# Optimization experiments

Hardware: AMD Instinct MI355X
Metric: run time of the kernel (lower is better)

Reference implementation:

```python
import jax, jax.numpy as jnp
import numpy as np
import math

B, S, IN_DIM = 4, 2048, 512
D, H, L, FF = 256, 4, 4, 2048
HD = D // H
EPS = 1e-5


def _pos_encoding(S, D, dtype=jnp.float32):
    pos = jnp.arange(S, dtype=jnp.float32)[:, None]
    div = jnp.exp(jnp.arange(0, D, 2, dtype=jnp.float32) * (-math.log(10000.0) / D))
    pe = jnp.zeros((S, D), dtype=jnp.float32)
    pe = pe.at[:, 0::2].set(jnp.sin(pos * div))
    pe = pe.at[:, 1::2].set(jnp.cos(pos * div))
    return pe.astype(dtype)


def _layernorm(x, w, b):
    mu = jnp.mean(x, axis=-1, keepdims=True)
    var = jnp.var(x, axis=-1, keepdims=True)
    return (x - mu) * jax.lax.rsqrt(var + EPS) * w + b


def setup_inputs() -> dict:
    key = jax.random.key(0)
    ks = jax.random.split(key, 12)
    sc = 0.02
    inp = {
        "x": jax.random.normal(ks[0], (B, S, IN_DIM), dtype=jnp.float32),
        "W_in": jax.random.normal(ks[1], (D, IN_DIM), dtype=jnp.float32) * sc,
        "b_in": jnp.zeros((D,), dtype=jnp.float32),
        "qkv_w": jax.random.normal(ks[2], (L, 3 * D, D), dtype=jnp.float32) * sc,
        "qkv_b": jnp.zeros((L, 3 * D), dtype=jnp.float32),
        "out_w": jax.random.normal(ks[3], (L, D, D), dtype=jnp.float32) * sc,
        "out_b": jnp.zeros((L, D), dtype=jnp.float32),
        "ln1_w": jnp.ones((L, D), dtype=jnp.float32),
        "ln1_b": jnp.zeros((L, D), dtype=jnp.float32),
        "ff1_w": jax.random.normal(ks[4], (L, FF, D), dtype=jnp.float32) * sc,
        "ff1_b": jnp.zeros((L, FF), dtype=jnp.float32),
        "ff2_w": jax.random.normal(ks[5], (L, D, FF), dtype=jnp.float32) * sc,
        "ff2_b": jnp.zeros((L, D), dtype=jnp.float32),
        "ln2_w": jnp.ones((L, D), dtype=jnp.float32),
        "ln2_b": jnp.zeros((L, D), dtype=jnp.float32),
        "W_fc": jax.random.normal(ks[6], (IN_DIM, D), dtype=jnp.float32) * sc,
        "b_fc": jnp.zeros((IN_DIM,), dtype=jnp.float32),
    }
    return inp


def reference(x, W_in, b_in, qkv_w, qkv_b, out_w, out_b, ln1_w, ln1_b,
              ff1_w, ff1_b, ff2_w, ff2_b, ln2_w, ln2_b, W_fc, b_fc):
    # input projection + positional encoding (dropout=0 / eval)
    h = jnp.einsum('bsi,di->bsd', x, W_in) + b_in
    h = h + _pos_encoding(S, D, h.dtype)[None]

    scale = 1.0 / math.sqrt(HD)
    for l in range(L):
        # --- self-attention (unfused: explicit QK^T + softmax + V) ---
        qkv = jnp.einsum('bsd,ed->bse', h, qkv_w[l]) + qkv_b[l]  # [B,S,3D]
        q, k, v = jnp.split(qkv, 3, axis=-1)
        q = q.reshape(B, S, H, HD).transpose(0, 2, 1, 3)  # [B,H,S,HD]
        k = k.reshape(B, S, H, HD).transpose(0, 2, 1, 3)
        v = v.reshape(B, S, H, HD).transpose(0, 2, 1, 3)
        scores = jnp.einsum('bhqd,bhkd->bhqk', q, k) * scale  # [B,H,S,S]
        attn = jax.nn.softmax(scores, axis=-1)
        ctx = jnp.einsum('bhqk,bhkd->bhqd', attn, v)
        ctx = ctx.transpose(0, 2, 1, 3).reshape(B, S, D)
        sa = jnp.einsum('bsd,ed->bse', ctx, out_w[l]) + out_b[l]
        h = _layernorm(h + sa, ln1_w[l], ln1_b[l])  # post-norm
        # --- feed-forward (relu) ---
        ff = jax.nn.relu(jnp.einsum('bsd,fd->bsf', h, ff1_w[l]) + ff1_b[l])
        ff = jnp.einsum('bsf,df->bsd', ff, ff2_w[l]) + ff2_b[l]
        h = _layernorm(h + ff, ln2_w[l], ln2_b[l])

    # final projection from last time step
    return jnp.einsum('bd,od->bo', h[:, -1, :], W_fc) + b_fc  # [B, IN_DIM]
```

## Files before the change

kernel.cpp:

```cpp
#include <hip/hip_runtime.h>
#include <math.h>

#define S_LEN 2048
#define DMODEL 256
#define NHEAD 4
#define HDIM 64
#define NLAYER 4
#define FFDIM 2048
#define INDIM 512
#define BATCH 4
#define NTOK (BATCH * S_LEN)
#define EPSV 1e-5f
#define KSPLIT 4

typedef __attribute__((ext_vector_type(8))) short frag8;
typedef __attribute__((ext_vector_type(4))) float f32x4v;
typedef unsigned short u16;
typedef unsigned int u32;

__device__ __forceinline__ float pe_val(int s, int d) {
    const float c = 0.035977892f;
    float dv = expf(-(float)(d & ~1) * c);
    float arg = (float)s * dv;
    return (d & 1) ? cosf(arg) : sinf(arg);
}

__device__ __forceinline__ u16 f2bf(float f) {
    union { float f; unsigned u; } v; v.f = f;
    unsigned r = v.u + 0x7fffu + ((v.u >> 16) & 1u);
    return (u16)(r >> 16);
}

__device__ __forceinline__ u32 pk2bf(float lo, float hi) {
    union { float f; u32 u; } a, b; a.f = lo; b.f = hi;
    return __builtin_amdgcn_perm(b.u, a.u, 0x07060302u);
}

__device__ __forceinline__ void load_lds16(const u16* g, u16* l) {
    __builtin_amdgcn_global_load_lds(
        (const __attribute__((address_space(1))) unsigned int*)g,
        (__attribute__((address_space(3))) unsigned int*)l, 16, 0, 0);
}


__global__ __launch_bounds__(256) void cvt_all(
    const float* __restrict__ x, const float* __restrict__ W_in,
    const float* __restrict__ qkv_w, const float* __restrict__ out_w,
    const float* __restrict__ ff1_w, const float* __restrict__ ff2_w,
    u16* __restrict__ xb, u16* __restrict__ W_in_b,
    u16* __restrict__ qkv_w_b, u16* __restrict__ out_w_b,
    u16* __restrict__ ff1_w_b, u16* __restrict__ ff2_w_b)
{
    const int i = blockIdx.x * 256 + threadIdx.x;
    const float* src; u16* dst; int base;
    if (i < 1048576)      { src = x;     dst = xb;      base = 0; }
    else if (i < 1081344) { src = W_in;  dst = W_in_b;  base = 1048576; }
    else if (i < 1277952) { src = qkv_w; dst = qkv_w_b; base = 1081344; }
    else if (i < 1343488) { src = out_w; dst = out_w_b; base = 1277952; }
    else if (i < 1867776) { src = ff1_w; dst = ff1_w_b; base = 1343488; }
    else                  { src = ff2_w; dst = ff2_w_b; base = 1867776; }
    const int e = (i - base) * 4;
    const float4 v = *(const float4*)(src + e);
    ushort4 o;
    o.x = f2bf(v.x); o.y = f2bf(v.y); o.z = f2bf(v.z); o.w = f2bf(v.w);
    *(ushort4*)(dst + e) = o;
}

template <int MODE>
__global__ __launch_bounds__(256) void gemm_mfma(
    const u16* __restrict__ A, const u16* __restrict__ W,
    const float* __restrict__ bias, u16* __restrict__ Cb,
    int M, int N, int K)
{
    __shared__ __align__(16) u16 As[128 * 32];
    __shared__ __align__(16) u16 Bs[128 * 32];
    const int t = threadIdx.x;
    const int w = t >> 6, lane = t & 63;
    const int col = lane & 15, quad = lane >> 4;
    const int qx = (quad ^ ((col >> 1) & 3)) * 8;
    const int m0 = blockIdx.x * 128, n0 = blockIdx.y * 128;
    const int wm = (w >> 1) * 64, wn = (w & 1) * 64;

    const int r0 = lane >> 2;
    const int kc = ((lane & 3) ^ ((lane >> 3) & 3)) * 8;
    const u16* pA0 = A + (size_t)(m0 + (w * 2 + 0) * 16 + r0) * K + kc;
    const u16* pA1 = A + (size_t)(m0 + (w * 2 + 1) * 16 + r0) * K + kc;
    const u16* pB0 = W + (size_t)(n0 + (w * 2 + 0) * 16 + r0) * K + kc;
    const u16* pB1 = W + (size_t)(n0 + (w * 2 + 1) * 16 + r0) * K + kc;
    u16* lA0 = As + (w * 2 + 0) * 512;
    u16* lA1 = As + (w * 2 + 1) * 512;
    u16* lB0 = Bs + (w * 2 + 0) * 512;
    u16* lB1 = Bs + (w * 2 + 1) * 512;

    f32x4v acc[4][4];
#pragma unroll
    for (int i = 0; i < 4; ++i)
#pragma unroll
        for (int j = 0; j < 4; ++j) acc[i][j] = (f32x4v){0.f, 0.f, 0.f, 0.f};

    for (int kb = 0; kb < K; kb += 32) {
        __syncthreads();
        load_lds16(pA0 + kb, lA0);
        load_lds16(pA1 + kb, lA1);
        load_lds16(pB0 + kb, lB0);
        load_lds16(pB1 + kb, lB1);
        __syncthreads();

        frag8 a[4], b[4];
#pragma unroll
        for (int i = 0; i < 4; ++i)
            a[i] = *(const frag8*)&As[(wm + i * 16 + col) * 32 + qx];
#pragma unroll
        for (int j = 0; j < 4; ++j)
            b[j] = *(const frag8*)&Bs[(wn + j * 16 + col) * 32 + qx];
#pragma unroll
        for (int i = 0; i < 4; ++i)
#pragma unroll
            for (int j = 0; j < 4; ++j)
                acc[i][j] = __builtin_amdgcn_mfma_f32_16x16x32_bf16(
                    a[i], b[j], acc[i][j], 0, 0, 0);
    }

#pragma unroll
    for (int j = 0; j < 4; ++j) {
        const int cn = n0 + wn + j * 16 + col;
        const float bv = bias[cn];
#pragma unroll
        for (int i = 0; i < 4; ++i) {
#pragma unroll
            for (int r = 0; r < 4; ++r) {
                const int cm = m0 + wm + i * 16 + quad * 4 + r;
                float v = acc[i][j][r] + bv;
                if (MODE == 2) v = fmaxf(v, 0.f);
                Cb[(size_t)cm * N + cn] = f2bf(v);
            }
        }
    }
}

template <int MODE>
__global__ __launch_bounds__(256) void gemm64(
    const u16* __restrict__ A, const u16* __restrict__ W,
    const float* __restrict__ bias,
    float* __restrict__ Cf, u16* __restrict__ Cb,
    int M, int N, int K)
{
    __shared__ __align__(16) u16 As[64 * 32];
    __shared__ __align__(16) u16 Bs[64 * 32];
    const int t = threadIdx.x;
    const int w = t >> 6, lane = t & 63;
    const int col = lane & 15, quad = lane >> 4;
    const int qx = (quad ^ ((col >> 1) & 3)) * 8;
    const int m0 = blockIdx.x * 64, n0 = blockIdx.y * 64;
    const int wm = (w >> 1) * 32, wn = (w & 1) * 32;

    const int r0 = lane >> 2;
    const int kc = ((lane & 3) ^ ((lane >> 3) & 3)) * 8;
    const u16* pA = A + (size_t)(m0 + w * 16 + r0) * K + kc;
    const u16* pB = W + (size_t)(n0 + w * 16 + r0) * K + kc;
    u16* lA = As + w * 512;
    u16* lB = Bs + w * 512;

    f32x4v acc[2][2];
#pragma unroll
    for (int i = 0; i < 2; ++i)
#pragma unroll
        for (int j = 0; j < 2; ++j) acc[i][j] = (f32x4v){0.f, 0.f, 0.f, 0.f};

    for (int kb = 0; kb < K; kb += 32) {
        __syncthreads();
        load_lds16(pA + kb, lA);
        load_lds16(pB + kb, lB);
        __syncthreads();

        frag8 a[2], b[2];
#pragma unroll
        for (int i = 0; i < 2; ++i)
            a[i] = *(const frag8*)&As[(wm + i * 16 + col) * 32 + qx];
#pragma unroll
        for (int j = 0; j < 2; ++j)
            b[j] = *(const frag8*)&Bs[(wn + j * 16 + col) * 32 + qx];
#pragma unroll
        for (int i = 0; i < 2; ++i)
#pragma unroll
            for (int j = 0; j < 2; ++j)
                acc[i][j] = __builtin_amdgcn_mfma_f32_16x16x32_bf16(
                    a[i], b[j], acc[i][j], 0, 0, 0);
    }

#pragma unroll
    for (int j = 0; j < 2; ++j) {
        const int cn = n0 + wn + j * 16 + col;
        const float bv = bias[cn];
#pragma unroll
        for (int i = 0; i < 2; ++i) {
#pragma unroll
            for (int r = 0; r < 4; ++r) {
                const int cm = m0 + wm + i * 16 + quad * 4 + r;
                float v = acc[i][j][r] + bv;
                if (MODE == 1) v += pe_val(cm & (S_LEN - 1), cn);
                Cf[(size_t)cm * N + cn] = v;
                if (MODE == 1) Cb[(size_t)cm * N + cn] = f2bf(v);
            }
        }
    }
}

#define PADW 72
__global__ __launch_bounds__(256) void vt_prep(const u16* __restrict__ qkv,
                                               u16* __restrict__ vt)
{
    __shared__ __align__(16) u16 Vl[64][PADW];
    const int t = threadIdx.x;
    const int bh = blockIdx.x, b = bh >> 2, hh = bh & 3;
    const int st = blockIdx.y;
    {
        const int row = t >> 2, seg = (t & 3) * 16;
        const u16* src = qkv + (size_t)(b * S_LEN + st * 64 + row) * 768
                         + 512 + hh * HDIM + seg;
        *(frag8*)&Vl[row][seg]     = *(const frag8*)src;
        *(frag8*)&Vl[row][seg + 8] = *(const frag8*)(src + 8);
    }
    __syncthreads();
    const int d = t >> 2, s0 = (t & 3) * 16;
    frag8 v0, v1;
#pragma unroll
    for (int i = 0; i < 8; ++i) v0[i] = (short)Vl[s0 + i][d];
#pragma unroll
    for (int i = 0; i < 8; ++i) v1[i] = (short)Vl[s0 + 8 + i][d];
    u16* dst = vt + ((size_t)bh * 64 + d) * S_LEN + st * 64 + s0;
    *(frag8*)dst = v0;
    *(frag8*)(dst + 8) = v1;
}

__global__ __launch_bounds__(256) void attn_part(const u16* __restrict__ qkv,
                                                 const u16* __restrict__ vt,
                                                 float* __restrict__ Opart,
                                                 float* __restrict__ lpart)
{
    __shared__ __align__(16) u16 Ks0[64 * 32], Ks1[64 * 32];
    __shared__ __align__(16) u16 Vt0[64 * 32], Vt1[64 * 32];
    __shared__ __align__(16) u16 Ps[4][2][2][512];

    const int t = threadIdx.x;
    const int w = t >> 6, lane = t & 63;
    const int col = lane & 15, quad = lane >> 4;
    const int sq = (col >> 1) & 3;
    const int qx = (quad ^ sq) * 8;
    const int bh = blockIdx.x, b = bh >> 2, hh = bh & 3;
    const int qt = blockIdx.y, ks = blockIdx.z;

    frag8 qf[2][2];
#pragma unroll
    for (int qg = 0; qg < 2; ++qg) {
        const int qrow = qt * 128 + w * 32 + qg * 16 + col;
        const u16* qp = qkv + (size_t)(b * S_LEN + qrow) * 768 + hh * HDIM;
        qf[qg][0] = *(const frag8*)(qp + quad * 8);
        qf[qg][1] = *(const frag8*)(qp + 32 + quad * 8);
    }

    f32x4v Oacc[2][4];
#pragma unroll
    for (int qg = 0; qg < 2; ++qg)
#pragma unroll
        for (int dt = 0; dt < 4; ++dt) Oacc[qg][dt] = (f32x4v){0.f, 0.f, 0.f, 0.f};
    float lsum[2] = {0.f, 0.f};
    const float SCL = 0.125f * 1.44269504f;

    const int srow = w * 16 + (lane >> 2);
    const int sseg = ((lane & 3) ^ ((lane >> 3) & 3)) * 8;
    const int kb0 = ks * (S_LEN / KSPLIT);
    const u16* kbase = qkv + (size_t)(b * S_LEN + kb0 + srow) * 768
                       + 256 + hh * HDIM + sseg;
    const u16* vbase = vt + ((size_t)bh * 64 + srow) * S_LEN + kb0 + sseg;
    u16* lK0 = Ks0 + w * 512;
    u16* lK1 = Ks1 + w * 512;
    u16* lV0 = Vt0 + w * 512;
    u16* lV1 = Vt1 + w * 512;

    for (int kt = 0; kt < S_LEN / KSPLIT / 64; ++kt) {
        __syncthreads();
        const u16* kp = kbase + (size_t)kt * 64 * 768;
        const u16* vp = vbase + kt * 64;
        load_lds16(kp, lK0);
        load_lds16(kp + 32, lK1);
        load_lds16(vp, lV0);
        load_lds16(vp + 32, lV1);
        __syncthreads();

#pragma unroll
        for (int nt = 0; nt < 4; ++nt) {
            const frag8 k0 = *(const frag8*)&Ks0[(nt * 16 + col) * 32 + qx];
            const frag8 k1 = *(const frag8*)&Ks1[(nt * 16 + col) * 32 + qx];
            const int c = (nt & 1) * 2 + (quad >> 1);
            const int poff = col * 32 + ((c ^ sq) * 8) + (quad & 1) * 4;
#pragma unroll
            for (int qg = 0; qg < 2; ++qg) {
                f32x4v s = (f32x4v){0.f, 0.f, 0.f, 0.f};
                s = __builtin_amdgcn_mfma_f32_16x16x32_bf16(k0, qf[qg][0], s, 0, 0, 0);
                s = __builtin_amdgcn_mfma_f32_16x16x32_bf16(k1, qf[qg][1], s, 0, 0, 0);
                const float p0 = exp2f(s[0] * SCL);
                const float p1 = exp2f(s[1] * SCL);
                const float p2 = exp2f(s[2] * SCL);
                const float p3 = exp2f(s[3] * SCL);
                lsum[qg] += (p0 + p1) + (p2 + p3);
                uint2 pk;
                pk.x = pk2bf(p0, p1);
                pk.y = pk2bf(p2, p3);
                *(uint2*)&Ps[w][qg][nt >> 1][poff] = pk;
            }
        }

        frag8 pf[2][2];
#pragma unroll
        for (int qg = 0; qg < 2; ++qg) {
            pf[qg][0] = *(const frag8*)&Ps[w][qg][0][col * 32 + qx];
            pf[qg][1] = *(const frag8*)&Ps[w][qg][1][col * 32 + qx];
        }
#pragma unroll
        for (int dt = 0; dt < 4; ++dt) {
            const frag8 v0 = *(const frag8*)&Vt0[(dt * 16 + col) * 32 + qx];
            const frag8 v1 = *(const frag8*)&Vt1[(dt * 16 + col) * 32 + qx];
#pragma unroll
            for (int qg = 0; qg < 2; ++qg) {
                Oacc[qg][dt] = __builtin_amdgcn_mfma_f32_16x16x32_bf16(
                    v0, pf[qg][0], Oacc[qg][dt], 0, 0, 0);
                Oacc[qg][dt] = __builtin_amdgcn_mfma_f32_16x16x32_bf16(
                    v1, pf[qg][1], Oacc[qg][dt], 0, 0, 0);
            }
        }
    }

#pragma unroll
    for (int qg = 0; qg < 2; ++qg) {
        float ls = lsum[qg];
        ls += __shfl_xor(ls, 16);
        ls += __shfl_xor(ls, 32);
        const int qrow = qt * 128 + w * 32 + qg * 16 + col;
        float* op = Opart + (((size_t)ks * 16 + bh) * S_LEN + qrow) * 64;
#pragma unroll
        for (int dt = 0; dt < 4; ++dt) {
            float4 o;
            o.x = Oacc[qg][dt][0]; o.y = Oacc[qg][dt][1];
            o.z = Oacc[qg][dt][2]; o.w = Oacc[qg][dt][3];
            *(float4*)(op + dt * 16 + quad * 4) = o;
        }
        if (quad == 0)
            lpart[((size_t)ks * 16 + bh) * S_LEN + qrow] = ls;
    }
}

__global__ __launch_bounds__(256) void attn_combine(const float* __restrict__ Opart,
                                                    const float* __restrict__ lpart,
                                                    u16* __restrict__ ctx)
{
    const int idx = blockIdx.x * 256 + threadIdx.x;
    const int d4 = idx & 15;
    const int q = (idx >> 4) & (S_LEN - 1);
    const int bh = idx >> 15;
    const int b = bh >> 2, hh = bh & 3;

    float4 o = {0.f, 0.f, 0.f, 0.f};
    float l = 0.f;
#pragma unroll
    for (int ks = 0; ks < KSPLIT; ++ks) {
        const float4 po = *(const float4*)&Opart[
            (((size_t)ks * 16 + bh) * S_LEN + q) * 64 + d4 * 4];
        o.x += po.x; o.y += po.y; o.z += po.z; o.w += po.w;
        l += lpart[((size_t)ks * 16 + bh) * S_LEN + q];
    }
    const float inv = 1.f / l;
    ushort4 r;
    r.x = f2bf(o.x * inv); r.y = f2bf(o.y * inv);
    r.z = f2bf(o.z * inv); r.w = f2bf(o.w * inv);
    *(ushort4*)&ctx[((size_t)(b * S_LEN + q)) * DMODEL + hh * HDIM + d4 * 4] = r;
}

__global__ __launch_bounds__(256) void add_ln(float* __restrict__ h,
                                              u16* __restrict__ hb,
                                              const float* __restrict__ r,
                                              const float* __restrict__ w,
                                              const float* __restrict__ b)
{
    const int t = blockIdx.x;
    const int d = threadIdx.x;
    const size_t idx = (size_t)t * DMODEL + d;
    const float x = h[idx] + r[idx];

    float s = x, s2 = x * x;
#pragma unroll
    for (int off = 32; off; off >>= 1) {
        s += __shfl_down(s, off);
        s2 += __shfl_down(s2, off);
    }
    __shared__ float ls[4], ls2[4];
    __shared__ float mu_s, rs_s;
    const int wid = d >> 6, lane = d & 63;
    if (lane == 0) { ls[wid] = s; ls2[wid] = s2; }
    __syncthreads();
    if (d == 0) {
        const float ts = ls[0] + ls[1] + ls[2] + ls[3];
        const float ts2 = ls2[0] + ls2[1] + ls2[2] + ls2[3];
        const float mu = ts * (1.f / DMODEL);
        const float var = ts2 * (1.f / DMODEL) - mu * mu;
        mu_s = mu;
        rs_s = rsqrtf(var + EPSV);
    }
    __syncthreads();
    const float y = (x - mu_s) * rs_s * w[d] + b[d];
    h[idx] = y;
    hb[idx] = f2bf(y);
}

__global__ __launch_bounds__(256) void final_proj(const float* __restrict__ h,
                                                  const float* __restrict__ Wfc,
                                                  const float* __restrict__ bfc,
                                                  float* __restrict__ out)
{
    const int idx = blockIdx.x * 256 + threadIdx.x;
    const int b = idx >> 9;
    const int o = idx & 511;
    const float* hp = h + (size_t)(b * S_LEN + S_LEN - 1) * DMODEL;
    const float* wp = Wfc + (size_t)o * DMODEL;
    float s = 0.f;
#pragma unroll 4
    for (int d = 0; d < DMODEL; ++d) s += hp[d] * wp[d];
    out[idx] = s + bfc[o];
}

extern "C" void kernel_launch(void* const* d_in, const int* in_sizes, int n_in,
                              void* d_out, int out_size, void* d_ws, size_t ws_size,
                              hipStream_t stream)
{
    const float* x     = (const float*)d_in[0];
    const float* W_in  = (const float*)d_in[1];
    const float* b_in  = (const float*)d_in[2];
    const float* qkv_w = (const float*)d_in[3];
    const float* qkv_b = (const float*)d_in[4];
    const float* out_w = (const float*)d_in[5];
    const float* out_b = (const float*)d_in[6];
    const float* ln1_w = (const float*)d_in[7];
    const float* ln1_b = (const float*)d_in[8];
    const float* ff1_w = (const float*)d_in[9];
    const float* ff1_b = (const float*)d_in[10];
    const float* ff2_w = (const float*)d_in[11];
    const float* ff2_b = (const float*)d_in[12];
    const float* ln2_w = (const float*)d_in[13];
    const float* ln2_b = (const float*)d_in[14];
    const float* W_fc  = (const float*)d_in[15];
    const float* b_fc  = (const float*)d_in[16];
    float* out = (float*)d_out;

    char* p = (char*)d_ws;
    float* h  = (float*)p; p += (size_t)NTOK * DMODEL * 4;
    float* sa = (float*)p; p += (size_t)NTOK * DMODEL * 4;
    u16* hb    = (u16*)p;  p += (size_t)NTOK * DMODEL * 2;
    u16* xb    = (u16*)p;  p += (size_t)NTOK * INDIM * 2;
    u16* qkvb  = (u16*)p;  p += (size_t)NTOK * 768 * 2;
    u16* ctxb  = (u16*)p;  p += (size_t)NTOK * DMODEL * 2;
    u16* ffb   = (u16*)p;  p += (size_t)NTOK * FFDIM * 2;
    u16* vtb   = (u16*)p;  p += (size_t)16 * 64 * S_LEN * 2;
    u16* W_in_b  = (u16*)p; p += (size_t)131072 * 2;
    u16* qkv_w_b = (u16*)p; p += (size_t)786432 * 2;
    u16* out_w_b = (u16*)p; p += (size_t)262144 * 2;
    u16* ff1_w_b = (u16*)p; p += (size_t)2097152 * 2;
    u16* ff2_w_b = (u16*)p; p += (size_t)2097152 * 2;
    if (ws_size < (size_t)94633984) return;

    float* Opart = (float*)ffb;
    float* lpart = sa;

    cvt_all<<<9344, 256, 0, stream>>>(x, W_in, qkv_w, out_w, ff1_w, ff2_w,
                                      xb, W_in_b, qkv_w_b, out_w_b, ff1_w_b, ff2_w_b);

    gemm64<1><<<dim3(NTOK / 64, DMODEL / 64), 256, 0, stream>>>(
        xb, W_in_b, b_in, h, hb, NTOK, DMODEL, INDIM);

    for (int l = 0; l < NLAYER; ++l) {
        gemm_mfma<0><<<dim3(NTOK / 128, 768 / 128), 256, 0, stream>>>(
            hb, qkv_w_b + (size_t)l * 768 * DMODEL, qkv_b + l * 768,
            qkvb, NTOK, 768, DMODEL);
        vt_prep<<<dim3(16, 32), 256, 0, stream>>>(qkvb, vtb);
        attn_part<<<dim3(BATCH * NHEAD, S_LEN / 128, KSPLIT), 256, 0, stream>>>(
            qkvb, vtb, Opart, lpart);
        attn_combine<<<2048, 256, 0, stream>>>(Opart, lpart, ctxb);
        gemm64<3><<<dim3(NTOK / 64, DMODEL / 64), 256, 0, stream>>>(
            ctxb, out_w_b + (size_t)l * DMODEL * DMODEL, out_b + l * DMODEL,
            sa, nullptr, NTOK, DMODEL, DMODEL);
        add_ln<<<NTOK, 256, 0, stream>>>(h, hb, sa, ln1_w + l * DMODEL, ln1_b + l * DMODEL);
        gemm_mfma<2><<<dim3(NTOK / 128, FFDIM / 128), 256, 0, stream>>>(
            hb, ff1_w_b + (size_t)l * FFDIM * DMODEL, ff1_b + l * FFDIM,
            ffb, NTOK, FFDIM, DMODEL);
        gemm64<3><<<dim3(NTOK / 64, DMODEL / 64), 256, 0, stream>>>(
            ffb, ff2_w_b + (size_t)l * DMODEL * FFDIM, ff2_b + l * DMODEL,
            sa, nullptr, NTOK, DMODEL, FFDIM);
        add_ln<<<NTOK, 256, 0, stream>>>(h, hb, sa, ln2_w + l * DMODEL, ln2_b + l * DMODEL);
    }

    final_proj<<<8, 256, 0, stream>>>(h, W_fc, b_fc, out);
}
```

Baseline: 630.1 us.

## Keep residual stream in bf16, fuse V transpose into QKV GEMM, deepen K tile

Drops the fp32 residual and sublayer buffers so the GEMM outputs, add+layernorm and final projection read and write only bf16. The V transpose moves into the QKV GEMM epilogue, which removes the separate vt_prep launch. The small-N GEMM now loads 64-wide K slices per barrier, which halves the sync count. Q is pre-scaled at load so the softmax can use the raw hardware exp2. In exchange the residual path loses precision because it accumulates in bf16 across all layers.

New measurement: 569.9 us. 1.11x faster.

```diff
diff --git a/kernel.cpp b/kernel.cpp
--- a/kernel.cpp
+++ b/kernel.cpp
@@ -30,18 +30,18 @@
     unsigned r = v.u + 0x7fffu + ((v.u >> 16) & 1u);
     return (u16)(r >> 16);
 }
-
+__device__ __forceinline__ float bf2f(u16 h) {
+    union { u32 u; float f; } v; v.u = (u32)h << 16; return v.f;
+}
 __device__ __forceinline__ u32 pk2bf(float lo, float hi) {
     union { float f; u32 u; } a, b; a.f = lo; b.f = hi;
     return __builtin_amdgcn_perm(b.u, a.u, 0x07060302u);
 }
-
 __device__ __forceinline__ void load_lds16(const u16* g, u16* l) {
     __builtin_amdgcn_global_load_lds(
         (const __attribute__((address_space(1))) unsigned int*)g,
         (__attribute__((address_space(3))) unsigned int*)l, 16, 0, 0);
 }
-
 
 __global__ __launch_bounds__(256) void cvt_all(
     const float* __restrict__ x, const float* __restrict__ W_in,
@@ -70,7 +70,7 @@
 __global__ __launch_bounds__(256) void gemm_mfma(
     const u16* __restrict__ A, const u16* __restrict__ W,
     const float* __restrict__ bias, u16* __restrict__ Cb,
-    int M, int N, int K)
+    u16* __restrict__ vt, int M, int N, int K)
 {
     __shared__ __align__(16) u16 As[128 * 32];
     __shared__ __align__(16) u16 Bs[128 * 32];
@@ -127,39 +127,53 @@
         const float bv = bias[cn];
 #pragma unroll
         for (int i = 0; i < 4; ++i) {
+            const int cmb = m0 + wm + i * 16 + quad * 4;
+            float vv[4];
 #pragma unroll
             for (int r = 0; r < 4; ++r) {
-                const int cm = m0 + wm + i * 16 + quad * 4 + r;
                 float v = acc[i][j][r] + bv;
                 if (MODE == 2) v = fmaxf(v, 0.f);
-                Cb[(size_t)cm * N + cn] = f2bf(v);
+                vv[r] = v;
+                Cb[(size_t)(cmb + r) * N + cn] = f2bf(v);
             }
+            if (MODE == 4 && cn >= 512) {
+                const int dg = cn - 512;
+                const int bh = (cmb >> 11) * 4 + (dg >> 6);
+                uint2 pk;
+                pk.x = ((u32)f2bf(vv[1]) << 16) | f2bf(vv[0]);
+                pk.y = ((u32)f2bf(vv[3]) << 16) | f2bf(vv[2]);
+                *(uint2*)&vt[((size_t)bh * 64 + (dg & 63)) * S_LEN + (cmb & 2047)] = pk;
+            }
         }
     }
 }
 
 template <int MODE>
-__global__ __launch_bounds__(256) void gemm64(
+__global__ __launch_bounds__(256) void gemm64k(
     const u16* __restrict__ A, const u16* __restrict__ W,
-    const float* __restrict__ bias,
-    float* __restrict__ Cf, u16* __restrict__ Cb,
+    const float* __restrict__ bias, u16* __restrict__ Cb,
     int M, int N, int K)
 {
-    __shared__ __align__(16) u16 As[64 * 32];
-    __shared__ __align__(16) u16 Bs[64 * 32];
+    __shared__ __align__(16) u16 As[64 * 64];
+    __shared__ __align__(16) u16 Bs[64 * 64];
     const int t = threadIdx.x;
     const int w = t >> 6, lane = t & 63;
     const int col = lane & 15, quad = lane >> 4;
-    const int qx = (quad ^ ((col >> 1) & 3)) * 8;
+    const int px0 = ((quad ^ (col & 7))) * 8;
+    const int px1 = px0 ^ 32;
     const int m0 = blockIdx.x * 64, n0 = blockIdx.y * 64;
     const int wm = (w >> 1) * 32, wn = (w & 1) * 32;
 
-    const int r0 = lane >> 2;
-    const int kc = ((lane & 3) ^ ((lane >> 3) & 3)) * 8;
-    const u16* pA = A + (size_t)(m0 + w * 16 + r0) * K + kc;
-    const u16* pB = W + (size_t)(n0 + w * 16 + r0) * K + kc;
-    u16* lA = As + w * 512;
-    u16* lB = Bs + w * 512;
+    const int sr = lane >> 3;
+    const int lc = ((lane & 7) ^ sr) * 8;
+    const u16* pA0 = A + (size_t)(m0 + w * 16 + sr) * K + lc;
+    const u16* pA1 = A + (size_t)(m0 + w * 16 + 8 + sr) * K + lc;
+    const u16* pB0 = W + (size_t)(n0 + w * 16 + sr) * K + lc;
+    const u16* pB1 = W + (size_t)(n0 + w * 16 + 8 + sr) * K + lc;
+    u16* lA0 = As + (w * 16) * 64;
+    u16* lA1 = As + (w * 16 + 8) * 64;
+    u16* lB0 = Bs + (w * 16) * 64;
+    u16* lB1 = Bs + (w * 16 + 8) * 64;
 
     f32x4v acc[2][2];
 #pragma unroll
@@ -167,25 +181,31 @@
 #pragma unroll
         for (int j = 0; j < 2; ++j) acc[i][j] = (f32x4v){0.f, 0.f, 0.f, 0.f};
 
-    for (int kb = 0; kb < K; kb += 32) {
-        __syncthreads();
-        load_lds16(pA + kb, lA);
-        load_lds16(pB + kb, lB);
-        __syncthreads();
-
-        frag8 a[2], b[2];
-#pragma unroll
-        for (int i = 0; i < 2; ++i)
-            a[i] = *(const frag8*)&As[(wm + i * 16 + col) * 32 + qx];
-#pragma unroll
-        for (int j = 0; j < 2; ++j)
-            b[j] = *(const frag8*)&Bs[(wn + j * 16 + col) * 32 + qx];
-#pragma unroll
-        for (int i = 0; i < 2; ++i)
+    for (int kb = 0; kb < K; kb += 64) {
+        __syncthreads();
+        load_lds16(pA0 + kb, lA0);
+        load_lds16(pA1 + kb, lA1);
+        load_lds16(pB0 + kb, lB0);
+        load_lds16(pB1 + kb, lB1);
+        __syncthreads();
+
+#pragma unroll
+        for (int kh = 0; kh < 2; ++kh) {
+            const int px = kh ? px1 : px0;
+            frag8 a[2], b[2];
+#pragma unroll
+            for (int i = 0; i < 2; ++i)
+                a[i] = *(const frag8*)&As[(wm + i * 16 + col) * 64 + px];
 #pragma unroll
             for (int j = 0; j < 2; ++j)
-                acc[i][j] = __builtin_amdgcn_mfma_f32_16x16x32_bf16(
-                    a[i], b[j], acc[i][j], 0, 0, 0);
+                b[j] = *(const frag8*)&Bs[(wn + j * 16 + col) * 64 + px];
+#pragma unroll
+            for (int i = 0; i < 2; ++i)
+#pragma unroll
+                for (int j = 0; j < 2; ++j)
+                    acc[i][j] = __builtin_amdgcn_mfma_f32_16x16x32_bf16(
+                        a[i], b[j], acc[i][j], 0, 0, 0);
+        }
     }
 
 #pragma unroll
@@ -199,38 +219,10 @@
                 const int cm = m0 + wm + i * 16 + quad * 4 + r;
                 float v = acc[i][j][r] + bv;
                 if (MODE == 1) v += pe_val(cm & (S_LEN - 1), cn);
-                Cf[(size_t)cm * N + cn] = v;
-                if (MODE == 1) Cb[(size_t)cm * N + cn] = f2bf(v);
+                Cb[(size_t)cm * N + cn] = f2bf(v);
             }
         }
     }
-}
-
-#define PADW 72
-__global__ __launch_bounds__(256) void vt_prep(const u16* __restrict__ qkv,
-                                               u16* __restrict__ vt)
-{
-    __shared__ __align__(16) u16 Vl[64][PADW];
-    const int t = threadIdx.x;
-    const int bh = blockIdx.x, b = bh >> 2, hh = bh & 3;
-    const int st = blockIdx.y;
-    {
-        const int row = t >> 2, seg = (t & 3) * 16;
-        const u16* src = qkv + (size_t)(b * S_LEN + st * 64 + row) * 768
-                         + 512 + hh * HDIM + seg;
-        *(frag8*)&Vl[row][seg]     = *(const frag8*)src;
-        *(frag8*)&Vl[row][seg + 8] = *(const frag8*)(src + 8);
-    }
-    __syncthreads();
-    const int d = t >> 2, s0 = (t & 3) * 16;
-    frag8 v0, v1;
-#pragma unroll
-    for (int i = 0; i < 8; ++i) v0[i] = (short)Vl[s0 + i][d];
-#pragma unroll
-    for (int i = 0; i < 8; ++i) v1[i] = (short)Vl[s0 + 8 + i][d];
-    u16* dst = vt + ((size_t)bh * 64 + d) * S_LEN + st * 64 + s0;
-    *(frag8*)dst = v0;
-    *(frag8*)(dst + 8) = v1;
 }
 
 __global__ __launch_bounds__(256) void attn_part(const u16* __restrict__ qkv,
@@ -250,13 +242,20 @@
     const int bh = blockIdx.x, b = bh >> 2, hh = bh & 3;
     const int qt = blockIdx.y, ks = blockIdx.z;
 
+    const float SCL = 0.125f * 1.44269504f;
+
     frag8 qf[2][2];
 #pragma unroll
     for (int qg = 0; qg < 2; ++qg) {
         const int qrow = qt * 128 + w * 32 + qg * 16 + col;
         const u16* qp = qkv + (size_t)(b * S_LEN + qrow) * 768 + hh * HDIM;
-        qf[qg][0] = *(const frag8*)(qp + quad * 8);
-        qf[qg][1] = *(const frag8*)(qp + 32 + quad * 8);
+        const frag8 r0 = *(const frag8*)(qp + quad * 8);
+        const frag8 r1 = *(const frag8*)(qp + 32 + quad * 8);
+#pragma unroll
+        for (int e = 0; e < 8; ++e) {
+            qf[qg][0][e] = (short)f2bf(bf2f((u16)r0[e]) * SCL);
+            qf[qg][1][e] = (short)f2bf(bf2f((u16)r1[e]) * SCL);
+        }
     }
 
     f32x4v Oacc[2][4];
@@ -265,7 +264,6 @@
 #pragma unroll
         for (int dt = 0; dt < 4; ++dt) Oacc[qg][dt] = (f32x4v){0.f, 0.f, 0.f, 0.f};
     float lsum[2] = {0.f, 0.f};
-    const float SCL = 0.125f * 1.44269504f;
 
     const int srow = w * 16 + (lane >> 2);
     const int sseg = ((lane & 3) ^ ((lane >> 3) & 3)) * 8;
@@ -299,10 +297,10 @@
                 f32x4v s = (f32x4v){0.f, 0.f, 0.f, 0.f};
                 s = __builtin_amdgcn_mfma_f32_16x16x32_bf16(k0, qf[qg][0], s, 0, 0, 0);
                 s = __builtin_amdgcn_mfma_f32_16x16x32_bf16(k1, qf[qg][1], s, 0, 0, 0);
-                const float p0 = exp2f(s[0] * SCL);
-                const float p1 = exp2f(s[1] * SCL);
-                const float p2 = exp2f(s[2] * SCL);
-                const float p3 = exp2f(s[3] * SCL);
+                const float p0 = __builtin_amdgcn_exp2f(s[0]);
+                const float p1 = __builtin_amdgcn_exp2f(s[1]);
+                const float p2 = __builtin_amdgcn_exp2f(s[2]);
+                const float p3 = __builtin_amdgcn_exp2f(s[3]);
                 lsum[qg] += (p0 + p1) + (p2 + p3);
                 uint2 pk;
                 pk.x = pk2bf(p0, p1);
@@ -376,16 +374,15 @@
     *(ushort4*)&ctx[((size_t)(b * S_LEN + q)) * DMODEL + hh * HDIM + d4 * 4] = r;
 }
 
-__global__ __launch_bounds__(256) void add_ln(float* __restrict__ h,
-                                              u16* __restrict__ hb,
-                                              const float* __restrict__ r,
+__global__ __launch_bounds__(256) void add_ln(u16* __restrict__ hb,
+                                              const u16* __restrict__ r,
                                               const float* __restrict__ w,
                                               const float* __restrict__ b)
 {
     const int t = blockIdx.x;
     const int d = threadIdx.x;
     const size_t idx = (size_t)t * DMODEL + d;
-    const float x = h[idx] + r[idx];
+    const float x = bf2f(hb[idx]) + bf2f(r[idx]);
 
     float s = x, s2 = x * x;
 #pragma unroll
@@ -407,12 +404,10 @@
         rs_s = rsqrtf(var + EPSV);
     }
     __syncthreads();
-    const float y = (x - mu_s) * rs_s * w[d] + b[d];
-    h[idx] = y;
-    hb[idx] = f2bf(y);
-}
-
-__global__ __launch_bounds__(256) void final_proj(const float* __restrict__ h,
+    hb[idx] = f2bf((x - mu_s) * rs_s * w[d] + b[d]);
+}
+
+__global__ __launch_bounds__(256) void final_proj(const u16* __restrict__ hb,
                                                   const float* __restrict__ Wfc,
                                                   const float* __restrict__ bfc,
                                                   float* __restrict__ out)
@@ -420,11 +415,11 @@
     const int idx = blockIdx.x * 256 + threadIdx.x;
     const int b = idx >> 9;
     const int o = idx & 511;
-    const float* hp = h + (size_t)(b * S_LEN + S_LEN - 1) * DMODEL;
+    const u16* hp = hb + (size_t)(b * S_LEN + S_LEN - 1) * DMODEL;
     const float* wp = Wfc + (size_t)o * DMODEL;
     float s = 0.f;
 #pragma unroll 4
-    for (int d = 0; d < DMODEL; ++d) s += hp[d] * wp[d];
+    for (int d = 0; d < DMODEL; ++d) s += bf2f(hp[d]) * wp[d];
     out[idx] = s + bfc[o];
 }
 
@@ -452,9 +447,8 @@
     float* out = (float*)d_out;
 
     char* p = (char*)d_ws;
-    float* h  = (float*)p; p += (size_t)NTOK * DMODEL * 4;
-    float* sa = (float*)p; p += (size_t)NTOK * DMODEL * 4;
     u16* hb    = (u16*)p;  p += (size_t)NTOK * DMODEL * 2;
+    u16* sab   = (u16*)p;  p += (size_t)NTOK * DMODEL * 2;
     u16* xb    = (u16*)p;  p += (size_t)NTOK * INDIM * 2;
     u16* qkvb  = (u16*)p;  p += (size_t)NTOK * 768 * 2;
     u16* ctxb  = (u16*)p;  p += (size_t)NTOK * DMODEL * 2;
@@ -465,37 +459,36 @@
     u16* out_w_b = (u16*)p; p += (size_t)262144 * 2;
     u16* ff1_w_b = (u16*)p; p += (size_t)2097152 * 2;
     u16* ff2_w_b = (u16*)p; p += (size_t)2097152 * 2;
-    if (ws_size < (size_t)94633984) return;
+    if (ws_size < (size_t)82051072) return;
 
     float* Opart = (float*)ffb;
-    float* lpart = sa;
+    float* lpart = (float*)sab;
 
     cvt_all<<<9344, 256, 0, stream>>>(x, W_in, qkv_w, out_w, ff1_w, ff2_w,
                                       xb, W_in_b, qkv_w_b, out_w_b, ff1_w_b, ff2_w_b);
 
-    gemm64<1><<<dim3(NTOK / 64, DMODEL / 64), 256, 0, stream>>>(
-        xb, W_in_b, b_in, h, hb, NTOK, DMODEL, INDIM);
+    gemm64k<1><<<dim3(NTOK / 64, DMODEL / 64), 256, 0, stream>>>(
+        xb, W_in_b, b_in, hb, NTOK, DMODEL, INDIM);
 
     for (int l = 0; l < NLAYER; ++l) {
-        gemm_mfma<0><<<dim3(NTOK / 128, 768 / 128), 256, 0, stream>>>(
+        gemm_mfma<4><<<dim3(NTOK / 128, 768 / 128), 256, 0, stream>>>(
             hb, qkv_w_b + (size_t)l * 768 * DMODEL, qkv_b + l * 768,
-            qkvb, NTOK, 768, DMODEL);
-        vt_prep<<<dim3(16, 32), 256, 0, stream>>>(qkvb, vtb);
+            qkvb, vtb, NTOK, 768, DMODEL);
         attn_part<<<dim3(BATCH * NHEAD, S_LEN / 128, KSPLIT), 256, 0, stream>>>(
             qkvb, vtb, Opart, lpart);
         attn_combine<<<2048, 256, 0, stream>>>(Opart, lpart, ctxb);
-        gemm64<3><<<dim3(NTOK / 64, DMODEL / 64), 256, 0, stream>>>(
+        gemm64k<0><<<dim3(NTOK / 64, DMODEL / 64), 256, 0, stream>>>(
             ctxb, out_w_b + (size_t)l * DMODEL * DMODEL, out_b + l * DMODEL,
-            sa, nullptr, NTOK, DMODEL, DMODEL);
-        add_ln<<<NTOK, 256, 0, stream>>>(h, hb, sa, ln1_w + l * DMODEL, ln1_b + l * DMODEL);
+            sab, NTOK, DMODEL, DMODEL);
+        add_ln<<<NTOK, 256, 0, stream>>>(hb, sab, ln1_w + l * DMODEL, ln1_b + l * DMODEL);
         gemm_mfma<2><<<dim3(NTOK / 128, FFDIM / 128), 256, 0, stream>>>(
             hb, ff1_w_b + (size_t)l * FFDIM * DMODEL, ff1_b + l * FFDIM,
-            ffb, NTOK, FFDIM, DMODEL);
-        gemm64<3><<<dim3(NTOK / 64, DMODEL / 64), 256, 0, stream>>>(
+            ffb, nullptr, NTOK, FFDIM, DMODEL);
+        gemm64k<0><<<dim3(NTOK / 64, DMODEL / 64), 256, 0, stream>>>(
             ffb, ff2_w_b + (size_t)l * DMODEL * FFDIM, ff2_b + l * DMODEL,
-            sa, nullptr, NTOK, DMODEL, FFDIM);
-        add_ln<<<NTOK, 256, 0, stream>>>(h, hb, sa, ln2_w + l * DMODEL, ln2_b + l * DMODEL);
-    }
-
-    final_proj<<<8, 256, 0, stream>>>(h, W_fc, b_fc, out);
-}
+            sab, NTOK, DMODEL, FFDIM);
+        add_ln<<<NTOK, 256, 0, stream>>>(hb, sab, ln2_w + l * DMODEL, ln2_b + l * DMODEL);
+    }
+
+    final_proj<<<8, 256, 0, stream>>>(hb, W_fc, b_fc, out);
+}
```
